# Kernel tuning notes

Measured on AMD Instinct MI355X. Metric: run time of the kernel, lower is better.

Reference implementation:

```python
import jax, jax.numpy as jnp
import numpy as np

N_HEAD = 16

def setup_inputs() -> dict:
    key = jax.random.key(0)
    k1, k2, k3 = jax.random.split(key, 3)
    B, T, C = 2, 2048, 1024
    x_norm_for_qk = jax.random.normal(k1, (B, T, C), dtype=jnp.float32)
    xt_current_for_v = jax.random.normal(k2, (B, T, C), dtype=jnp.float32)
    W_attn = jax.random.normal(k3, (C, 2 * C), dtype=jnp.float32) * (1.0 / np.sqrt(C))
    b_attn = jnp.zeros((2 * C,), dtype=jnp.float32)
    return {"x_norm_for_qk": x_norm_for_qk, "xt_current_for_v": xt_current_for_v,
            "W_attn": W_attn, "b_attn": b_attn}

def reference(x_norm_for_qk, xt_current_for_v, W_attn, b_attn):
    B, T, C = x_norm_for_qk.shape
    H = N_HEAD
    D = C // H  # head dim
    qk = x_norm_for_qk @ W_attn + b_attn          # [B,T,2C]
    q, k = qk[..., :C], qk[..., C:]
    q = q.reshape(B, T, H, D).transpose(0, 2, 1, 3)   # [B,H,T,D]
    k = k.reshape(B, T, H, D).transpose(0, 2, 1, 3)
    v = xt_current_for_v.reshape(B, T, H, D).transpose(0, 2, 1, 3)
    scale = 1.0 / np.sqrt(D).astype(np.float32)
    scores = jnp.einsum('bhqd,bhkd->bhqk', q, k) * scale  # [B,H,T,T]
    causal = jnp.tril(jnp.ones((T, T), dtype=bool))
    scores = jnp.where(causal[None, None], scores, jnp.float32(-jnp.inf))
    weights = jax.nn.softmax(scores, axis=-1)  # dropout p=0.0 -> identity
    y = jnp.einsum('bhqk,bhkd->bhqd', weights, v)
    return y.transpose(0, 2, 1, 3).reshape(B, T, C)
```

## Files before the change

kernel.cpp:

```cpp
#include <hip/hip_runtime.h>
#include <hip/hip_bf16.h>
#include <math.h>

typedef __attribute__((ext_vector_type(8))) short s8v;
typedef __attribute__((ext_vector_type(4))) float f4v;
typedef unsigned short ush;
typedef unsigned int u32;

static __device__ __forceinline__ ush f2bf(float f) {
    u32 x = __builtin_bit_cast(u32, f);
    return (ush)((x + 0x7fffu + ((x >> 16) & 1u)) >> 16);
}
static __device__ __forceinline__ u32 bfpack(float lo, float hi) {
    u32 a = __builtin_bit_cast(u32, lo) + 0x8000u;
    u32 b = __builtin_bit_cast(u32, hi) + 0x8000u;
    return __builtin_amdgcn_perm(b, a, 0x07060302);
}
static __device__ __forceinline__ void gl_lds16(const void* g, void* l) {
    __builtin_amdgcn_global_load_lds(
        (const __attribute__((address_space(1))) u32*)g,
        (__attribute__((address_space(3))) u32*)l, 16, 0, 0);
}

__global__ __launch_bounds__(256) void xb_kernel(
    const float* __restrict__ X, ush* __restrict__ Xb)
{
    const size_t i = ((size_t)blockIdx.x * 256 + threadIdx.x) * 8;
    float4 v0 = *(const float4*)(X + i);
    float4 v1 = *(const float4*)(X + i + 4);
    uint4 o;
    o.x = bfpack(v0.x, v0.y); o.y = bfpack(v0.z, v0.w);
    o.z = bfpack(v1.x, v1.y); o.w = bfpack(v1.z, v1.w);
    *(uint4*)(Xb + i) = o;
}

__global__ __launch_bounds__(256) void wt_kernel(
    const float* __restrict__ W, ush* __restrict__ Wt)
{
    __shared__ float Ts[64][68];
    const int tid = threadIdx.x;
    const int n0 = blockIdx.x * 64;
    const int k0 = blockIdx.y * 64;
    #pragma unroll
    for (int p = 0; p < 4; ++p) {
        const int idx = p * 256 + tid;
        const int kr = idx >> 4, nc4 = idx & 15;
        float4 v = *(const float4*)(W + (size_t)(k0 + kr) * 2048 + n0 + nc4 * 4);
        Ts[kr][nc4 * 4 + 0] = v.x; Ts[kr][nc4 * 4 + 1] = v.y;
        Ts[kr][nc4 * 4 + 2] = v.z; Ts[kr][nc4 * 4 + 3] = v.w;
    }
    __syncthreads();
    const int n = tid >> 2, kb = (tid & 3) * 16;
    #pragma unroll
    for (int p = 0; p < 4; ++p) {
        const int k = kb + p * 4;
        ushort4 o;
        o.x = f2bf(Ts[k + 0][n]); o.y = f2bf(Ts[k + 1][n]);
        o.z = f2bf(Ts[k + 2][n]); o.w = f2bf(Ts[k + 3][n]);
        *(ushort4*)(Wt + (size_t)(n0 + n) * 1024 + k0 + k) = o;
    }
}

__global__ __launch_bounds__(256) void vt_kernel(
    const float* __restrict__ XV, ush* __restrict__ Vt)
{
    __shared__ float Ts[64][68];
    const int tid = threadIdx.x;
    const int t0 = blockIdx.x * 64;
    const int bh = blockIdx.y;
    const int b = bh >> 4, h = bh & 15;
    #pragma unroll
    for (int p = 0; p < 4; ++p) {
        const int idx = p * 256 + tid;
        const int tr = idx >> 4, dc4 = idx & 15;
        float4 v = *(const float4*)(XV + (size_t)(b * 2048 + t0 + tr) * 1024
                                    + h * 64 + dc4 * 4);
        Ts[tr][dc4 * 4 + 0] = v.x; Ts[tr][dc4 * 4 + 1] = v.y;
        Ts[tr][dc4 * 4 + 2] = v.z; Ts[tr][dc4 * 4 + 3] = v.w;
    }
    __syncthreads();
    const int d = tid >> 2, tb = (tid & 3) * 16;
    #pragma unroll
    for (int p = 0; p < 4; ++p) {
        const int tq = tb + p * 4;
        ushort4 o;
        o.x = f2bf(Ts[tq + 0][d]); o.y = f2bf(Ts[tq + 1][d]);
        o.z = f2bf(Ts[tq + 2][d]); o.w = f2bf(Ts[tq + 3][d]);
        *(ushort4*)(Vt + (size_t)((b * 16 + h) * 64 + d) * 2048 + t0 + tq) = o;
    }
}

__global__ __launch_bounds__(256) void gemm_kernel(
    const ush* __restrict__ Xb, const ush* __restrict__ Wt,
    const float* __restrict__ bias,
    ush* __restrict__ Qb, ush* __restrict__ Kb)
{
    __shared__ ush As[128 * 32];
    __shared__ ush Bs[128 * 32];

    const int tid = threadIdx.x;
    const int wid = tid >> 6, lane = tid & 63;
    const int quad = lane >> 4, l15 = lane & 15;
    const int wm = wid >> 1, wn = wid & 1;
    const int m0 = blockIdx.y * 128, n0 = blockIdx.x * 128;

    const int lrow = lane >> 2;
    const int lkk = (lane & 3) * 8;
    const size_t arow = (size_t)(m0 + wid * 32 + lrow);
    const size_t brow = (size_t)(n0 + wid * 32 + lrow);
    ush* AsW = &As[wid * 1024];
    ush* BsW = &Bs[wid * 1024];

    f4v acc[4][4];
    #pragma unroll
    for (int i = 0; i < 4; ++i)
        #pragma unroll
        for (int j = 0; j < 4; ++j) acc[i][j] = (f4v){0.f, 0.f, 0.f, 0.f};

    for (int k0 = 0; k0 < 1024; k0 += 32) {
        gl_lds16(Xb + arow * 1024 + k0 + lkk, AsW);
        gl_lds16(Xb + (arow + 16) * 1024 + k0 + lkk, AsW + 512);
        gl_lds16(Wt + brow * 1024 + k0 + lkk, BsW);
        gl_lds16(Wt + (brow + 16) * 1024 + k0 + lkk, BsW + 512);
        __syncthreads();

        s8v a[4], bf[4];
        #pragma unroll
        for (int i = 0; i < 4; ++i)
            a[i] = *(const s8v*)&As[(wm * 64 + i * 16 + l15) * 32 + quad * 8];
        #pragma unroll
        for (int j = 0; j < 4; ++j)
            bf[j] = *(const s8v*)&Bs[(wn * 64 + j * 16 + l15) * 32 + quad * 8];
        #pragma unroll
        for (int i = 0; i < 4; ++i)
            #pragma unroll
            for (int j = 0; j < 4; ++j)
                acc[i][j] = __builtin_amdgcn_mfma_f32_16x16x32_bf16(
                    a[i], bf[j], acc[i][j], 0, 0, 0);
        __syncthreads();
    }

    #pragma unroll
    for (int j = 0; j < 4; ++j) {
        const int n = n0 + wn * 64 + j * 16 + l15;
        const float bv = bias[n];
        const bool is_k = n >= 1024;
        const int nn = n & 1023;
        const int h = nn >> 6, d = nn & 63;
        ush* dst = is_k ? Kb : Qb;
        #pragma unroll
        for (int i = 0; i < 4; ++i) {
            const int mrow = m0 + wm * 64 + i * 16 + quad * 4;
            #pragma unroll
            for (int r = 0; r < 4; ++r) {
                const int m = mrow + r;
                const int b = m >> 11, t = m & 2047;
                float val = acc[i][j][r] + bv;
                if (!is_k) val *= 0.125f;
                dst[(size_t)((b * 16 + h) * 2048 + t) * 64 + d] = f2bf(val);
            }
        }
    }
}

__global__ __launch_bounds__(256) void attn_kernel(
    const ush* __restrict__ Qb, const ush* __restrict__ Kb,
    const ush* __restrict__ Vt, float* __restrict__ Y)
{
    __shared__ ush Qs[64 * 72];
    __shared__ ush Ks[64 * 72];
    __shared__ ush Vs[64 * 72];

    const int tid = threadIdx.x;
    const int w = tid >> 6, lane = tid & 63;
    const int quad = lane >> 4, l15 = lane & 15;
    const int bh = blockIdx.x;
    const int b = bh >> 4, h = bh & 15;
    const int qt = gridDim.y - 1 - blockIdx.y;
    const int q0 = qt * 64;

    const ush* Qg = Qb + (size_t)bh * 2048 * 64;
    const ush* Kg = Kb + (size_t)bh * 2048 * 64;
    const ush* Vg = Vt + (size_t)bh * 64 * 2048;

    const int srow = tid >> 3;
    const int sc = (tid & 7) * 8;

    {
        uint4 qa = *(const uint4*)(Qg + (size_t)(q0 + srow) * 64 + sc);
        uint4 qb2 = *(const uint4*)(Qg + (size_t)(q0 + srow + 32) * 64 + sc);
        uint4 ka = *(const uint4*)(Kg + (size_t)srow * 64 + sc);
        uint4 kb2 = *(const uint4*)(Kg + (size_t)(srow + 32) * 64 + sc);
        uint4 va = *(const uint4*)(Vg + (size_t)srow * 2048 + sc);
        uint4 vb = *(const uint4*)(Vg + (size_t)(srow + 32) * 2048 + sc);
        *(uint4*)&Qs[srow * 72 + sc] = qa;
        *(uint4*)&Qs[(srow + 32) * 72 + sc] = qb2;
        *(uint4*)&Ks[srow * 72 + sc] = ka;
        *(uint4*)&Ks[(srow + 32) * 72 + sc] = kb2;
        *(uint4*)&Vs[srow * 72 + sc] = va;
        *(uint4*)&Vs[(srow + 32) * 72 + sc] = vb;
    }
    __syncthreads();

    s8v bq[2];
    #pragma unroll
    for (int s = 0; s < 2; ++s)
        bq[s] = *(const s8v*)&Qs[(w * 16 + l15) * 72 + s * 32 + quad * 8];
    __syncthreads();

    ush* Psw = &Qs[w * 16 * 72];

    f4v acco[4];
    #pragma unroll
    for (int e = 0; e < 4; ++e) acco[e] = (f4v){0.f, 0.f, 0.f, 0.f};
    float mr = -INFINITY, lr = 0.f;

    for (int kt = 0; kt <= qt; ++kt) {
        const bool pf = kt < qt;
        uint4 ka, kb2, va, vb;
        if (pf) {
            const int kn = (kt + 1) * 64;
            ka = *(const uint4*)(Kg + (size_t)(kn + srow) * 64 + sc);
            kb2 = *(const uint4*)(Kg + (size_t)(kn + srow + 32) * 64 + sc);
            va = *(const uint4*)(Vg + (size_t)srow * 2048 + kn + sc);
            vb = *(const uint4*)(Vg + (size_t)(srow + 32) * 2048 + kn + sc);
        }

        f4v sacc[4];
        #pragma unroll
        for (int j = 0; j < 4; ++j) sacc[j] = (f4v){0.f, 0.f, 0.f, 0.f};
        #pragma unroll
        for (int s = 0; s < 2; ++s) {
            #pragma unroll
            for (int j = 0; j < 4; ++j) {
                s8v ak = *(const s8v*)&Ks[(j * 16 + l15) * 72 + s * 32 + quad * 8];
                sacc[j] = __builtin_amdgcn_mfma_f32_16x16x32_bf16(
                    ak, bq[s], sacc[j], 0, 0, 0);
            }
        }

        float sv[4][4];
        #pragma unroll
        for (int j = 0; j < 4; ++j)
            #pragma unroll
            for (int r = 0; r < 4; ++r) sv[j][r] = sacc[j][r];
        if (kt == qt) {
            #pragma unroll
            for (int j = 0; j < 4; ++j)
                #pragma unroll
                for (int r = 0; r < 4; ++r)
                    if (j * 16 + quad * 4 + r > w * 16 + l15)
                        sv[j][r] = -INFINITY;
        }

        float mloc = sv[0][0];
        #pragma unroll
        for (int j = 0; j < 4; ++j)
            #pragma unroll
            for (int r = 0; r < 4; ++r) mloc = fmaxf(mloc, sv[j][r]);
        mloc = fmaxf(mloc, __shfl_xor(mloc, 16));
        mloc = fmaxf(mloc, __shfl_xor(mloc, 32));
        const float mnew = fmaxf(mr, mloc);
        const float alpha = __expf(mr - mnew);
        mr = mnew;

        float pe[4][4], ps = 0.f;
        #pragma unroll
        for (int j = 0; j < 4; ++j)
            #pragma unroll
            for (int r = 0; r < 4; ++r) {
                pe[j][r] = __expf(sv[j][r] - mnew);
                ps += pe[j][r];
            }
        ps += __shfl_xor(ps, 16);
        ps += __shfl_xor(ps, 32);
        lr = lr * alpha + ps;

        #pragma unroll
        for (int j = 0; j < 4; ++j) {
            uint2 pk;
            pk.x = bfpack(pe[j][0], pe[j][1]);
            pk.y = bfpack(pe[j][2], pe[j][3]);
            *(uint2*)&Psw[l15 * 72 + j * 16 + quad * 4] = pk;
        }

        #pragma unroll
        for (int r = 0; r < 4; ++r) {
            const float av = __shfl(alpha, quad * 4 + r, 16);
            #pragma unroll
            for (int e = 0; e < 4; ++e) acco[e][r] *= av;
        }

        #pragma unroll
        for (int s = 0; s < 2; ++s) {
            s8v ap = *(const s8v*)&Psw[l15 * 72 + s * 32 + quad * 8];
            #pragma unroll
            for (int e = 0; e < 4; ++e) {
                s8v bv = *(const s8v*)&Vs[(e * 16 + l15) * 72 + s * 32 + quad * 8];
                acco[e] = __builtin_amdgcn_mfma_f32_16x16x32_bf16(
                    ap, bv, acco[e], 0, 0, 0);
            }
        }

        __syncthreads();
        if (pf) {
            *(uint4*)&Ks[srow * 72 + sc] = ka;
            *(uint4*)&Ks[(srow + 32) * 72 + sc] = kb2;
            *(uint4*)&Vs[srow * 72 + sc] = va;
            *(uint4*)&Vs[(srow + 32) * 72 + sc] = vb;
            __syncthreads();
        }
    }

    #pragma unroll
    for (int r = 0; r < 4; ++r) {
        const float lv = __shfl(lr, quad * 4 + r, 16);
        const float inv = 1.0f / lv;
        const int q = q0 + w * 16 + quad * 4 + r;
        #pragma unroll
        for (int e = 0; e < 4; ++e) {
            const int d = e * 16 + l15;
            Y[(size_t)(b * 2048 + q) * 1024 + h * 64 + d] = acco[e][r] * inv;
        }
    }
}

extern "C" void kernel_launch(void* const* d_in, const int* in_sizes, int n_in,
                              void* d_out, int out_size, void* d_ws,
                              size_t ws_size, hipStream_t stream)
{
    const float* x_qk = (const float*)d_in[0];
    const float* x_v  = (const float*)d_in[1];
    const float* W    = (const float*)d_in[2];
    const float* bias = (const float*)d_in[3];
    float* out = (float*)d_out;

    unsigned char* ws = (unsigned char*)d_ws;
    ush* Xb = (ush*)(ws);
    ush* Vt = (ush*)(ws);
    ush* Wt = (ush*)(ws + (8u << 20));
    ush* Qb = (ush*)(ws + (12u << 20));
    ush* Kb = (ush*)(ws + (20u << 20));

    xb_kernel<<<2048, 256, 0, stream>>>(x_qk, Xb);
    wt_kernel<<<dim3(32, 16), 256, 0, stream>>>(W, Wt);
    gemm_kernel<<<dim3(16, 32), 256, 0, stream>>>(Xb, Wt, bias, Qb, Kb);
    vt_kernel<<<dim3(32, 32), 256, 0, stream>>>(x_v, Vt);
    attn_kernel<<<dim3(32, 32), 256, 0, stream>>>(Qb, Kb, Vt, out);
}
```

Baseline: 166.6 us.

## Rewrite attention with 32x32 MFMA, async LDS double-buffering, exp2 softmax; fuse prep kernels

The attention kernel now handles 128-query tiles with 32 rows per wave and uses 32x32x16 bf16 MFMAs. K/V tiles are double-buffered through global_load_lds into XOR-swizzled LDS, and the softmax uses exp2 with log2e folded into the Q scale. Output goes through an LDS transpose so stores are coalesced float4. The grid is remapped to pair heavy and light causal tiles, and the X-cast and W-transpose kernels are merged into one launch. These changes target MFMA issue efficiency, load latency, and launch overhead, at the cost of more registers and LDS per block.

```diff
diff --git a/kernel.cpp b/kernel.cpp
--- a/kernel.cpp
+++ b/kernel.cpp
@@ -4,8 +4,11 @@
 
 typedef __attribute__((ext_vector_type(8))) short s8v;
 typedef __attribute__((ext_vector_type(4))) float f4v;
+typedef __attribute__((ext_vector_type(16))) float f16v;
 typedef unsigned short ush;
 typedef unsigned int u32;
+
+#define QSCALE 0.180336880f
 
 static __device__ __forceinline__ ush f2bf(float f) {
     u32 x = __builtin_bit_cast(u32, f);
@@ -21,43 +24,48 @@
         (const __attribute__((address_space(1))) u32*)g,
         (__attribute__((address_space(3))) u32*)l, 16, 0, 0);
 }
-
-__global__ __launch_bounds__(256) void xb_kernel(
-    const float* __restrict__ X, ush* __restrict__ Xb)
-{
-    const size_t i = ((size_t)blockIdx.x * 256 + threadIdx.x) * 8;
-    float4 v0 = *(const float4*)(X + i);
-    float4 v1 = *(const float4*)(X + i + 4);
-    uint4 o;
-    o.x = bfpack(v0.x, v0.y); o.y = bfpack(v0.z, v0.w);
-    o.z = bfpack(v1.x, v1.y); o.w = bfpack(v1.z, v1.w);
-    *(uint4*)(Xb + i) = o;
-}
-
-__global__ __launch_bounds__(256) void wt_kernel(
-    const float* __restrict__ W, ush* __restrict__ Wt)
+#if __has_builtin(__builtin_amdgcn_exp2f)
+#define EXP2F(x) __builtin_amdgcn_exp2f(x)
+#else
+#define EXP2F(x) exp2f(x)
+#endif
+
+__global__ __launch_bounds__(256) void prepA_kernel(
+    const float* __restrict__ X, const float* __restrict__ W,
+    ush* __restrict__ Xb, ush* __restrict__ Wt)
 {
     __shared__ float Ts[64][68];
     const int tid = threadIdx.x;
-    const int n0 = blockIdx.x * 64;
-    const int k0 = blockIdx.y * 64;
-    #pragma unroll
-    for (int p = 0; p < 4; ++p) {
-        const int idx = p * 256 + tid;
-        const int kr = idx >> 4, nc4 = idx & 15;
-        float4 v = *(const float4*)(W + (size_t)(k0 + kr) * 2048 + n0 + nc4 * 4);
-        Ts[kr][nc4 * 4 + 0] = v.x; Ts[kr][nc4 * 4 + 1] = v.y;
-        Ts[kr][nc4 * 4 + 2] = v.z; Ts[kr][nc4 * 4 + 3] = v.w;
-    }
-    __syncthreads();
-    const int n = tid >> 2, kb = (tid & 3) * 16;
-    #pragma unroll
-    for (int p = 0; p < 4; ++p) {
-        const int k = kb + p * 4;
-        ushort4 o;
-        o.x = f2bf(Ts[k + 0][n]); o.y = f2bf(Ts[k + 1][n]);
-        o.z = f2bf(Ts[k + 2][n]); o.w = f2bf(Ts[k + 3][n]);
-        *(ushort4*)(Wt + (size_t)(n0 + n) * 1024 + k0 + k) = o;
+    const int bid = blockIdx.x;
+    if (bid < 2048) {
+        const size_t i = ((size_t)bid * 256 + tid) * 8;
+        float4 v0 = *(const float4*)(X + i);
+        float4 v1 = *(const float4*)(X + i + 4);
+        uint4 o;
+        o.x = bfpack(v0.x, v0.y); o.y = bfpack(v0.z, v0.w);
+        o.z = bfpack(v1.x, v1.y); o.w = bfpack(v1.z, v1.w);
+        *(uint4*)(Xb + i) = o;
+    } else {
+        const int id = bid - 2048;
+        const int n0 = (id & 31) * 64, k0 = (id >> 5) * 64;
+        #pragma unroll
+        for (int p = 0; p < 4; ++p) {
+            const int idx = p * 256 + tid;
+            const int kr = idx >> 4, nc4 = idx & 15;
+            float4 v = *(const float4*)(W + (size_t)(k0 + kr) * 2048 + n0 + nc4 * 4);
+            Ts[kr][nc4 * 4 + 0] = v.x; Ts[kr][nc4 * 4 + 1] = v.y;
+            Ts[kr][nc4 * 4 + 2] = v.z; Ts[kr][nc4 * 4 + 3] = v.w;
+        }
+        __syncthreads();
+        const int n = tid >> 2, kb = (tid & 3) * 16;
+        #pragma unroll
+        for (int p = 0; p < 4; ++p) {
+            const int k = kb + p * 4;
+            ushort4 o;
+            o.x = f2bf(Ts[k + 0][n]); o.y = f2bf(Ts[k + 1][n]);
+            o.z = f2bf(Ts[k + 2][n]); o.w = f2bf(Ts[k + 3][n]);
+            *(ushort4*)(Wt + (size_t)(n0 + n) * 1024 + k0 + k) = o;
+        }
     }
 }
 
@@ -156,172 +164,156 @@
                 const int m = mrow + r;
                 const int b = m >> 11, t = m & 2047;
                 float val = acc[i][j][r] + bv;
-                if (!is_k) val *= 0.125f;
+                if (!is_k) val *= QSCALE;
                 dst[(size_t)((b * 16 + h) * 2048 + t) * 64 + d] = f2bf(val);
             }
         }
     }
 }
 
-__global__ __launch_bounds__(256) void attn_kernel(
+__global__ __launch_bounds__(256, 2) void attn_kernel(
     const ush* __restrict__ Qb, const ush* __restrict__ Kb,
     const ush* __restrict__ Vt, float* __restrict__ Y)
 {
-    __shared__ ush Qs[64 * 72];
-    __shared__ ush Ks[64 * 72];
-    __shared__ ush Vs[64 * 72];
+    __shared__ ush SMEM[25600];
+    ush* Kbuf = SMEM;
+    ush* Vbuf = SMEM + 8192;
+    ush* Pq   = SMEM + 16384;
 
     const int tid = threadIdx.x;
     const int w = tid >> 6, lane = tid & 63;
-    const int quad = lane >> 4, l15 = lane & 15;
-    const int bh = blockIdx.x;
+    const int l31 = lane & 31, hi = lane >> 5;
+
+    const int idx = blockIdx.x;
+    const int half = idx >> 8, pair = idx & 255;
+    const int qt = half ? (pair & 15) : 15 - (pair & 15);
+    const int bh = (pair >> 4) + half * 16;
     const int b = bh >> 4, h = bh & 15;
-    const int qt = gridDim.y - 1 - blockIdx.y;
-    const int q0 = qt * 64;
+    const int q0 = qt * 128;
+    const int ktmax = 2 * qt + 1;
 
     const ush* Qg = Qb + (size_t)bh * 2048 * 64;
     const ush* Kg = Kb + (size_t)bh * 2048 * 64;
     const ush* Vg = Vt + (size_t)bh * 64 * 2048;
 
-    const int srow = tid >> 3;
-    const int sc = (tid & 7) * 8;
+    ush* Pw = Pq + w * 2304;
 
     {
-        uint4 qa = *(const uint4*)(Qg + (size_t)(q0 + srow) * 64 + sc);
-        uint4 qb2 = *(const uint4*)(Qg + (size_t)(q0 + srow + 32) * 64 + sc);
-        uint4 ka = *(const uint4*)(Kg + (size_t)srow * 64 + sc);
-        uint4 kb2 = *(const uint4*)(Kg + (size_t)(srow + 32) * 64 + sc);
-        uint4 va = *(const uint4*)(Vg + (size_t)srow * 2048 + sc);
-        uint4 vb = *(const uint4*)(Vg + (size_t)(srow + 32) * 2048 + sc);
-        *(uint4*)&Qs[srow * 72 + sc] = qa;
-        *(uint4*)&Qs[(srow + 32) * 72 + sc] = qb2;
-        *(uint4*)&Ks[srow * 72 + sc] = ka;
-        *(uint4*)&Ks[(srow + 32) * 72 + sc] = kb2;
-        *(uint4*)&Vs[srow * 72 + sc] = va;
-        *(uint4*)&Vs[(srow + 32) * 72 + sc] = vb;
-    }
+        const int r8 = lane >> 3, c8 = lane & 7;
+        #pragma unroll
+        for (int p = 0; p < 4; ++p) {
+            const int row = p * 8 + r8;
+            uint4 v = *(const uint4*)(Qg + (size_t)(q0 + w * 32 + row) * 64 + c8 * 8);
+            *(uint4*)&Pw[row * 72 + c8 * 8] = v;
+        }
+    }
+    s8v bq[4];
+    #pragma unroll
+    for (int s = 0; s < 4; ++s)
+        bq[s] = *(const s8v*)&Pw[l31 * 72 + s * 16 + hi * 8];
+
+    const int r8 = lane >> 3;
+    const int g8 = ((lane & 7) ^ r8) * 8;
+    auto stage = [&](int kt, int buf) {
+        const int k0e = kt * 64;
+        const ush* kg = Kg + (size_t)(k0e + w * 16 + r8) * 64 + g8;
+        gl_lds16(kg, &Kbuf[buf * 4096 + (w * 16) * 64]);
+        gl_lds16(kg + 8 * 64, &Kbuf[buf * 4096 + (w * 16 + 8) * 64]);
+        const ush* vg = Vg + (size_t)(w * 16 + r8) * 2048 + k0e + g8;
+        gl_lds16(vg, &Vbuf[buf * 4096 + (w * 16) * 64]);
+        gl_lds16(vg + 8 * 2048, &Vbuf[buf * 4096 + (w * 16 + 8) * 64]);
+    };
+
+    f16v acco0 = {}, acco1 = {};
+    float mr = -INFINITY, lr = 0.f;
+    const int qg = q0 + w * 32 + l31;
+
+    stage(0, 0);
     __syncthreads();
 
-    s8v bq[2];
-    #pragma unroll
-    for (int s = 0; s < 2; ++s)
-        bq[s] = *(const s8v*)&Qs[(w * 16 + l15) * 72 + s * 32 + quad * 8];
-    __syncthreads();
-
-    ush* Psw = &Qs[w * 16 * 72];
-
-    f4v acco[4];
-    #pragma unroll
-    for (int e = 0; e < 4; ++e) acco[e] = (f4v){0.f, 0.f, 0.f, 0.f};
-    float mr = -INFINITY, lr = 0.f;
-
-    for (int kt = 0; kt <= qt; ++kt) {
-        const bool pf = kt < qt;
-        uint4 ka, kb2, va, vb;
-        if (pf) {
-            const int kn = (kt + 1) * 64;
-            ka = *(const uint4*)(Kg + (size_t)(kn + srow) * 64 + sc);
-            kb2 = *(const uint4*)(Kg + (size_t)(kn + srow + 32) * 64 + sc);
-            va = *(const uint4*)(Vg + (size_t)srow * 2048 + kn + sc);
-            vb = *(const uint4*)(Vg + (size_t)(srow + 32) * 2048 + kn + sc);
-        }
-
-        f4v sacc[4];
-        #pragma unroll
-        for (int j = 0; j < 4; ++j) sacc[j] = (f4v){0.f, 0.f, 0.f, 0.f};
-        #pragma unroll
-        for (int s = 0; s < 2; ++s) {
-            #pragma unroll
-            for (int j = 0; j < 4; ++j) {
-                s8v ak = *(const s8v*)&Ks[(j * 16 + l15) * 72 + s * 32 + quad * 8];
-                sacc[j] = __builtin_amdgcn_mfma_f32_16x16x32_bf16(
-                    ak, bq[s], sacc[j], 0, 0, 0);
+    for (int kt = 0; kt <= ktmax; ++kt) {
+        const int buf = kt & 1;
+        if (kt < ktmax) stage(kt + 1, buf ^ 1);
+
+        f16v s0 = {}, s1 = {};
+        #pragma unroll
+        for (int s = 0; s < 4; ++s) {
+            const int ch = (s << 1) + hi;
+            const int row0 = l31, row1 = 32 + l31;
+            s8v ak0 = *(const s8v*)&Kbuf[buf * 4096 + row0 * 64 + ((ch ^ (row0 & 7)) << 3)];
+            s8v ak1 = *(const s8v*)&Kbuf[buf * 4096 + row1 * 64 + ((ch ^ (row1 & 7)) << 3)];
+            s0 = __builtin_amdgcn_mfma_f32_32x32x16_bf16(ak0, bq[s], s0, 0, 0, 0);
+            s1 = __builtin_amdgcn_mfma_f32_32x32x16_bf16(ak1, bq[s], s1, 0, 0, 0);
+        }
+
+        const bool needmask = (kt * 64 + 63) > (q0 + w * 32);
+        float mloc = -INFINITY;
+        #pragma unroll
+        for (int r = 0; r < 16; ++r) {
+            float v0 = s0[r], v1 = s1[r];
+            if (needmask) {
+                const int keyb = kt * 64 + (r & 3) + 8 * (r >> 2) + 4 * hi;
+                if (keyb > qg) v0 = -INFINITY;
+                if (keyb + 32 > qg) v1 = -INFINITY;
+                s0[r] = v0; s1[r] = v1;
             }
-        }
-
-        float sv[4][4];
-        #pragma unroll
-        for (int j = 0; j < 4; ++j)
-            #pragma unroll
-            for (int r = 0; r < 4; ++r) sv[j][r] = sacc[j][r];
-        if (kt == qt) {
-            #pragma unroll
-            for (int j = 0; j < 4; ++j)
-                #pragma unroll
-                for (int r = 0; r < 4; ++r)
-                    if (j * 16 + quad * 4 + r > w * 16 + l15)
-                        sv[j][r] = -INFINITY;
-        }
-
-        float mloc = sv[0][0];
-        #pragma unroll
-        for (int j = 0; j < 4; ++j)
-            #pragma unroll
-            for (int r = 0; r < 4; ++r) mloc = fmaxf(mloc, sv[j][r]);
-        mloc = fmaxf(mloc, __shfl_xor(mloc, 16));
+            mloc = fmaxf(mloc, fmaxf(v0, v1));
+        }
         mloc = fmaxf(mloc, __shfl_xor(mloc, 32));
         const float mnew = fmaxf(mr, mloc);
-        const float alpha = __expf(mr - mnew);
+        const float alpha = EXP2F(mr - mnew);
         mr = mnew;
 
-        float pe[4][4], ps = 0.f;
-        #pragma unroll
-        for (int j = 0; j < 4; ++j)
-            #pragma unroll
-            for (int r = 0; r < 4; ++r) {
-                pe[j][r] = __expf(sv[j][r] - mnew);
-                ps += pe[j][r];
-            }
-        ps += __shfl_xor(ps, 16);
+        float ps = 0.f;
+        #pragma unroll
+        for (int g4 = 0; g4 < 4; ++g4) {
+            float e0a = EXP2F(s0[g4 * 4 + 0] - mnew), e0b = EXP2F(s0[g4 * 4 + 1] - mnew);
+            float e0c = EXP2F(s0[g4 * 4 + 2] - mnew), e0d = EXP2F(s0[g4 * 4 + 3] - mnew);
+            float e1a = EXP2F(s1[g4 * 4 + 0] - mnew), e1b = EXP2F(s1[g4 * 4 + 1] - mnew);
+            float e1c = EXP2F(s1[g4 * 4 + 2] - mnew), e1d = EXP2F(s1[g4 * 4 + 3] - mnew);
+            ps += (e0a + e0b) + (e0c + e0d) + (e1a + e1b) + (e1c + e1d);
+            uint2 p0; p0.x = bfpack(e0a, e0b); p0.y = bfpack(e0c, e0d);
+            uint2 p1; p1.x = bfpack(e1a, e1b); p1.y = bfpack(e1c, e1d);
+            const int off = g4 * 8 + hi * 4;
+            *(uint2*)&Pw[l31 * 72 + off] = p0;
+            *(uint2*)&Pw[l31 * 72 + 32 + off] = p1;
+        }
         ps += __shfl_xor(ps, 32);
         lr = lr * alpha + ps;
 
         #pragma unroll
-        for (int j = 0; j < 4; ++j) {
-            uint2 pk;
-            pk.x = bfpack(pe[j][0], pe[j][1]);
-            pk.y = bfpack(pe[j][2], pe[j][3]);
-            *(uint2*)&Psw[l15 * 72 + j * 16 + quad * 4] = pk;
-        }
-
-        #pragma unroll
-        for (int r = 0; r < 4; ++r) {
-            const float av = __shfl(alpha, quad * 4 + r, 16);
-            #pragma unroll
-            for (int e = 0; e < 4; ++e) acco[e][r] *= av;
-        }
-
-        #pragma unroll
-        for (int s = 0; s < 2; ++s) {
-            s8v ap = *(const s8v*)&Psw[l15 * 72 + s * 32 + quad * 8];
-            #pragma unroll
-            for (int e = 0; e < 4; ++e) {
-                s8v bv = *(const s8v*)&Vs[(e * 16 + l15) * 72 + s * 32 + quad * 8];
-                acco[e] = __builtin_amdgcn_mfma_f32_16x16x32_bf16(
-                    ap, bv, acco[e], 0, 0, 0);
-            }
+        for (int r = 0; r < 16; ++r) { acco0[r] *= alpha; acco1[r] *= alpha; }
+
+        #pragma unroll
+        for (int s = 0; s < 4; ++s) {
+            s8v pf = *(const s8v*)&Pw[l31 * 72 + s * 16 + hi * 8];
+            const int ch = (s << 1) + hi;
+            const int row0 = l31, row1 = 32 + l31;
+            s8v av0 = *(const s8v*)&Vbuf[buf * 4096 + row0 * 64 + ((ch ^ (row0 & 7)) << 3)];
+            s8v av1 = *(const s8v*)&Vbuf[buf * 4096 + row1 * 64 + ((ch ^ (row1 & 7)) << 3)];
+            acco0 = __builtin_amdgcn_mfma_f32_32x32x16_bf16(av0, pf, acco0, 0, 0, 0);
+            acco1 = __builtin_amdgcn_mfma_f32_32x32x16_bf16(av1, pf, acco1, 0, 0, 0);
         }
 
         __syncthreads();
-        if (pf) {
-            *(uint4*)&Ks[srow * 72 + sc] = ka;
-            *(uint4*)&Ks[(srow + 32) * 72 + sc] = kb2;
-            *(uint4*)&Vs[srow * 72 + sc] = va;
-            *(uint4*)&Vs[(srow + 32) * 72 + sc] = vb;
-            __syncthreads();
-        }
-    }
-
-    #pragma unroll
-    for (int r = 0; r < 4; ++r) {
-        const float lv = __shfl(lr, quad * 4 + r, 16);
-        const float inv = 1.0f / lv;
-        const int q = q0 + w * 16 + quad * 4 + r;
-        #pragma unroll
-        for (int e = 0; e < 4; ++e) {
-            const int d = e * 16 + l15;
-            Y[(size_t)(b * 2048 + q) * 1024 + h * 64 + d] = acco[e][r] * inv;
-        }
+    }
+
+    __syncthreads();
+    float* LTw = (float*)SMEM + w * (32 * 68);
+    const float inv = 1.0f / lr;
+    #pragma unroll
+    for (int r = 0; r < 16; ++r) {
+        const int d = (r & 3) + 8 * (r >> 2) + 4 * hi;
+        LTw[l31 * 68 + d] = acco0[r] * inv;
+        LTw[l31 * 68 + 32 + d] = acco1[r] * inv;
+    }
+    const int qr4 = lane >> 4, chk = lane & 15;
+    #pragma unroll
+    for (int p = 0; p < 8; ++p) {
+        const int qrow = p * 4 + qr4;
+        f4v v = *(const f4v*)&LTw[qrow * 68 + chk * 4];
+        *(float4*)(Y + (size_t)(b * 2048 + q0 + w * 32 + qrow) * 1024
+                   + h * 64 + chk * 4) = (float4){v[0], v[1], v[2], v[3]};
     }
 }
 
@@ -342,9 +334,8 @@
     ush* Qb = (ush*)(ws + (12u << 20));
     ush* Kb = (ush*)(ws + (20u << 20));
 
-    xb_kernel<<<2048, 256, 0, stream>>>(x_qk, Xb);
-    wt_kernel<<<dim3(32, 16), 256, 0, stream>>>(W, Wt);
+    prepA_kernel<<<2560, 256, 0, stream>>>(x_qk, W, Xb, Wt);
     gemm_kernel<<<dim3(16, 32), 256, 0, stream>>>(Xb, Wt, bias, Qb, Kb);
     vt_kernel<<<dim3(32, 32), 256, 0, stream>>>(x_v, Vt);
-    attn_kernel<<<dim3(32, 32), 256, 0, stream>>>(Qb, Kb, Vt, out);
-}
+    attn_kernel<<<512, 256, 0, stream>>>(Qb, Kb, Vt, out);
+}
```

New measurement: 162.5 us. -2.4%, faster.
